# Performance work log

Measured on AMD Instinct MI355X. Metric: run time of the kernel, lower is better.

## Reference

```python
import jax, jax.numpy as jnp
import numpy as np

N_C, N_E, IN_FEAT, OUT_FEAT = 8192, 8192, 256, 128


def setup_inputs() -> dict:
    key = jax.random.key(0)
    ks = jax.random.split(key, 9)
    s = 1.0 / np.sqrt(IN_FEAT)
    return {
        "emb_cause": jax.random.normal(ks[0], (N_C, IN_FEAT), jnp.float32),
        "emb_effect": jax.random.normal(ks[1], (N_E, IN_FEAT), jnp.float32),
        "causal_mask": jax.random.randint(ks[2], (N_C, N_E), 0, 2, jnp.int32),
        "Wq": jax.random.uniform(ks[3], (IN_FEAT, OUT_FEAT), jnp.float32, -s, s),
        "bq": jax.random.uniform(ks[4], (OUT_FEAT,), jnp.float32, -s, s),
        "Wk": jax.random.uniform(ks[5], (IN_FEAT, OUT_FEAT), jnp.float32, -s, s),
        "bk": jax.random.uniform(ks[6], (OUT_FEAT,), jnp.float32, -s, s),
        "Wv": jax.random.uniform(ks[7], (IN_FEAT, OUT_FEAT), jnp.float32, -s, s),
        "bv": jax.random.uniform(ks[8], (OUT_FEAT,), jnp.float32, -s, s),
    }


def reference(emb_cause, emb_effect, causal_mask, Wq, bq, Wk, bk, Wv, bv):
    Q = emb_cause @ Wq + bq          # [N_c, D]
    K = emb_effect @ Wk + bk         # [N_e, D]
    V = emb_effect @ Wv + bv         # [N_e, D]
    scale = 1.0 / jnp.sqrt(jnp.asarray(Q.shape[-1], Q.dtype))
    scores = (Q @ K.T) * scale       # [N_c, N_e]
    scores = jnp.where(causal_mask == 0, -jnp.inf, scores)
    attn_weights = jax.nn.softmax(scores, axis=-1)
    causal_output = attn_weights @ V  # [N_c, D]
    return causal_output, attn_weights
```

## Files before the change

kernel.cpp:

```cpp
#include <hip/hip_runtime.h>

#define NC   8192
#define NEFF 8192
#define DIN  256
#define DOUT 128
#define SCALE 0.08838834764831843f

typedef float  f32x4  __attribute__((ext_vector_type(4)));
typedef short  s16x8  __attribute__((ext_vector_type(8)));
typedef unsigned long long u64;

__device__ __forceinline__ short f2bf(float f) {
    unsigned int u = __builtin_bit_cast(unsigned int, f);
    u += 0x7FFFu + ((u >> 16) & 1u);
    return (short)(u >> 16);
}

__device__ __forceinline__ s16x8 ld8(const short* p) {
    return *(const s16x8*)__builtin_assume_aligned(p, 16);
}

__device__ __forceinline__ unsigned getdw(int4 v, int i) {
    switch (i & 3) {
        case 0: return (unsigned)v.x;
        case 1: return (unsigned)v.y;
        case 2: return (unsigned)v.z;
        default: return (unsigned)v.w;
    }
}


__global__ __launch_bounds__(256, 2) void qkv_kernel(
    const float* __restrict__ embc, const float* __restrict__ embe,
    const float* __restrict__ Wq, const float* __restrict__ bq,
    const float* __restrict__ Wk, const float* __restrict__ bk,
    const float* __restrict__ Wv, const float* __restrict__ bv,
    short* __restrict__ Qf, short* __restrict__ Kf, short* __restrict__ Vf)
{
    const int mat = blockIdx.y;
    const float* src  = (mat == 0) ? embc : embe;
    const float* W    = (mat == 0) ? Wq : (mat == 1 ? Wk : Wv);
    const float* bias = (mat == 0) ? bq : (mat == 1 ? bk : bv);

    __shared__ short wt[DOUT][136];
    __shared__ short tbuf[4][16][132];
    __shared__ short tbufV[128][68];

    const int tid  = threadIdx.x;
    const int wave = tid >> 6, lane = tid & 63;
    const int quad = lane >> 4, ln16 = lane & 15;
    const int rowbase = blockIdx.x * 64;
    const int arow = rowbase + wave * 16 + ln16;

    f32x4 acc[8];
#pragma unroll
    for (int i = 0; i < 8; i++) acc[i] = (f32x4){0.f, 0.f, 0.f, 0.f};

    for (int h = 0; h < 2; h++) {
        __syncthreads();
        {
            const int n0 = (tid & 31) * 4;
            const int kb = tid >> 5;
#pragma unroll
            for (int i = 0; i < 16; i++) {
                const int k = kb + i * 8;
                const float4 w4 = *(const float4*)(W + (size_t)(h * 128 + k) * DOUT + n0);
                wt[n0 + 0][k] = f2bf(w4.x);
                wt[n0 + 1][k] = f2bf(w4.y);
                wt[n0 + 2][k] = f2bf(w4.z);
                wt[n0 + 3][k] = f2bf(w4.w);
            }
        }
        __syncthreads();

        s16x8 afr[4];
#pragma unroll
        for (int kc = 0; kc < 4; kc++) {
            const float* ap = src + (size_t)arow * DIN + h * 128 + kc * 32 + quad * 8;
            const float4 a0 = *(const float4*)ap;
            const float4 a1 = *(const float4*)(ap + 4);
            s16x8 a;
            a[0] = f2bf(a0.x); a[1] = f2bf(a0.y); a[2] = f2bf(a0.z); a[3] = f2bf(a0.w);
            a[4] = f2bf(a1.x); a[5] = f2bf(a1.y); a[6] = f2bf(a1.z); a[7] = f2bf(a1.w);
            afr[kc] = a;
        }
#pragma unroll
        for (int nt = 0; nt < 8; nt++) {
#pragma unroll
            for (int kc = 0; kc < 4; kc++) {
                const s16x8 b = ld8(&wt[nt * 16 + ln16][kc * 32 + quad * 8]);
                acc[nt] = __builtin_amdgcn_mfma_f32_16x16x32_bf16(afr[kc], b, acc[nt], 0, 0, 0);
            }
        }
    }

    if (mat < 2) {
        short* dst = (mat == 0) ? Qf : Kf;
        const float sc = (mat == 0) ? SCALE : 1.0f;
#pragma unroll
        for (int nt = 0; nt < 8; nt++) {
            const float bb = bias[nt * 16 + ln16];
#pragma unroll
            for (int r = 0; r < 4; r++)
                tbuf[wave][quad * 4 + r][nt * 16 + ln16] = f2bf((acc[nt][r] + bb) * sc);
        }
        const int tile = blockIdx.x * 4 + wave;
#pragma unroll
        for (int kc = 0; kc < 4; kc++) {
            const s16x8 fr = ld8(&tbuf[wave][ln16][kc * 32 + quad * 8]);
            *(s16x8*)(dst + ((size_t)(tile * 4 + kc) * 64 + lane) * 8) = fr;
        }
    } else {
#pragma unroll
        for (int nt = 0; nt < 8; nt++) {
            const float bb = bias[nt * 16 + ln16];
#pragma unroll
            for (int r = 0; r < 4; r++)
                tbufV[nt * 16 + ln16][wave * 16 + quad * 4 + r] = f2bf(acc[nt][r] + bb);
        }
        __syncthreads();
        const int ct = blockIdx.x >> 1;
        const int ksub0 = (blockIdx.x & 1) * 2;
        const int ks = wave & 1;
#pragma unroll
        for (int t = 0; t < 4; t++) {
            const int nt2 = (wave >> 1) * 4 + t;
            const s16x8 fr = ld8(&tbufV[nt2 * 16 + ln16][ks * 32 + quad * 8]);
            *(s16x8*)(Vf + ((size_t)((ct * 8 + nt2) * 4 + ksub0 + ks) * 64 + lane) * 8) = fr;
        }
    }
}

__global__ __launch_bounds__(256, 2) void stats_kernel(
    const int* __restrict__ mask, const short* __restrict__ Qf,
    const short* __restrict__ Kf, float* __restrict__ lsum,
    unsigned int* __restrict__ bm)
{
    __shared__ int4 bmbuf[4][32];

    const int bx = blockIdx.x, strip = blockIdx.y;
    const int tid  = threadIdx.x;
    const int wave = tid >> 6, lane = tid & 63;
    const int quad = lane >> 4, ln16 = lane & 15;
    const int rowbase = bx * 128 + wave * 32;
    const int t0 = rowbase >> 4;

    s16x8 aq[2][4];
#pragma unroll
    for (int rs = 0; rs < 2; rs++)
#pragma unroll
        for (int kc = 0; kc < 4; kc++)
            aq[rs][kc] = ld8(Qf + ((size_t)((t0 + rs) * 4 + kc) * 64 + lane) * 8);

    float lp[8] = {0.f, 0.f, 0.f, 0.f, 0.f, 0.f, 0.f, 0.f};

    for (int it = 0; it < 8; it++) {
        const int cb = strip * 1024 + it * 128;

        int4 mybm = {0, 0, 0, 0};
#pragma unroll 4
        for (int rr = 0; rr < 32; rr++) {
            const int* mrow = mask + (size_t)(rowbase + rr) * NEFF + cb;
            const int p0 = mrow[lane];
            const int p1 = mrow[64 + lane];
            const u64 b0 = __ballot(p0 != 0);
            const u64 b1 = __ballot(p1 != 0);
            int4 v;
            v.x = (int)(unsigned)(b0 & 0xffffffffull);
            v.y = (int)(unsigned)(b0 >> 32);
            v.z = (int)(unsigned)(b1 & 0xffffffffull);
            v.w = (int)(unsigned)(b1 >> 32);
            if (rr == lane) mybm = v;
        }
        if (lane < 32) {
            *(int4*)(bm + (size_t)(rowbase + lane) * 256 + (cb >> 5)) = mybm;
            bmbuf[wave][lane] = mybm;
        }
        int4 bmv[2][4];
#pragma unroll
        for (int rs = 0; rs < 2; rs++)
#pragma unroll
            for (int r = 0; r < 4; r++)
                bmv[rs][r] = bmbuf[wave][rs * 16 + quad * 4 + r];

#pragma unroll
        for (int nt = 0; nt < 8; nt++) {
            s16x8 bq[4];
#pragma unroll
            for (int kc = 0; kc < 4; kc++)
                bq[kc] = ld8(Kf + ((size_t)(((cb >> 4) + nt) * 4 + kc) * 64 + lane) * 8);
            f32x4 c0 = (f32x4){0.f, 0.f, 0.f, 0.f};
            f32x4 c1 = (f32x4){0.f, 0.f, 0.f, 0.f};
#pragma unroll
            for (int kc = 0; kc < 4; kc++) {
                c0 = __builtin_amdgcn_mfma_f32_16x16x32_bf16(aq[0][kc], bq[kc], c0, 0, 0, 0);
                c1 = __builtin_amdgcn_mfma_f32_16x16x32_bf16(aq[1][kc], bq[kc], c1, 0, 0, 0);
            }
#pragma unroll
            for (int rs = 0; rs < 2; rs++)
#pragma unroll
                for (int r = 0; r < 4; r++) {
                    const unsigned d = getdw(bmv[rs][r], nt >> 1);
                    const float cv = rs ? c1[r] : c0[r];
                    if ((d >> ((nt & 1) * 16 + ln16)) & 1u)
                        lp[rs * 4 + r] += __expf(cv);
                }
        }
    }

#pragma unroll
    for (int i = 0; i < 8; i++) {
        float v = lp[i];
        v += __shfl_xor(v, 1); v += __shfl_xor(v, 2);
        v += __shfl_xor(v, 4); v += __shfl_xor(v, 8);
        if (ln16 == 0)
            atomicAdd(&lsum[rowbase + (i >> 2) * 16 + quad * 4 + (i & 3)], v);
    }
}

__global__ __launch_bounds__(256, 2) void attn_kernel(
    const short* __restrict__ Qf, const short* __restrict__ Kf,
    const short* __restrict__ Vf, const float* __restrict__ lsum,
    const unsigned int* __restrict__ bm,
    float* __restrict__ outO, float* __restrict__ outW)
{
    __shared__ short wlds[4][32][132];

    const int bx = blockIdx.x, strip = blockIdx.y;
    const int tid  = threadIdx.x;
    const int wave = tid >> 6, lane = tid & 63;
    const int quad = lane >> 4, ln16 = lane & 15;
    const int rowbase = bx * 128 + wave * 32;
    const int t0 = rowbase >> 4;

    s16x8 aq[2][4];
#pragma unroll
    for (int rs = 0; rs < 2; rs++)
#pragma unroll
        for (int kc = 0; kc < 4; kc++)
            aq[rs][kc] = ld8(Qf + ((size_t)((t0 + rs) * 4 + kc) * 64 + lane) * 8);

    float rl[2][4];
#pragma unroll
    for (int rs = 0; rs < 2; rs++)
#pragma unroll
        for (int r = 0; r < 4; r++)
            rl[rs][r] = 1.0f / lsum[rowbase + rs * 16 + quad * 4 + r];

    f32x4 o[2][8];
#pragma unroll
    for (int rs = 0; rs < 2; rs++)
#pragma unroll
        for (int i = 0; i < 8; i++) o[rs][i] = (f32x4){0.f, 0.f, 0.f, 0.f};

    for (int it = 0; it < 8; it++) {
        const int cb = strip * 1024 + it * 128;

        int4 bmv[2][4];
#pragma unroll
        for (int rs = 0; rs < 2; rs++)
#pragma unroll
            for (int r = 0; r < 4; r++)
                bmv[rs][r] = *(const int4*)(bm + (size_t)(rowbase + rs * 16 + quad * 4 + r) * 256 + (cb >> 5));

#pragma unroll
        for (int nt = 0; nt < 8; nt++) {
            s16x8 bq[4];
#pragma unroll
            for (int kc = 0; kc < 4; kc++)
                bq[kc] = ld8(Kf + ((size_t)(((cb >> 4) + nt) * 4 + kc) * 64 + lane) * 8);
            f32x4 c0 = (f32x4){0.f, 0.f, 0.f, 0.f};
            f32x4 c1 = (f32x4){0.f, 0.f, 0.f, 0.f};
#pragma unroll
            for (int kc = 0; kc < 4; kc++) {
                c0 = __builtin_amdgcn_mfma_f32_16x16x32_bf16(aq[0][kc], bq[kc], c0, 0, 0, 0);
                c1 = __builtin_amdgcn_mfma_f32_16x16x32_bf16(aq[1][kc], bq[kc], c1, 0, 0, 0);
            }
#pragma unroll
            for (int rs = 0; rs < 2; rs++)
#pragma unroll
                for (int r = 0; r < 4; r++) {
                    const int row = rowbase + rs * 16 + quad * 4 + r;
                    const unsigned d = getdw(bmv[rs][r], nt >> 1);
                    const float cv = rs ? c1[r] : c0[r];
                    const float wv = ((d >> ((nt & 1) * 16 + ln16)) & 1u)
                                         ? __expf(cv) * rl[rs][r] : 0.0f;
                    outW[(size_t)row * NEFF + cb + nt * 16 + ln16] = wv;
                    wlds[wave][rs * 16 + quad * 4 + r][nt * 16 + ln16] = f2bf(wv);
                }
        }

#pragma unroll
        for (int ks = 0; ks < 4; ks++) {
            const s16x8 aw0 = ld8(&wlds[wave][ln16][ks * 32 + quad * 8]);
            const s16x8 aw1 = ld8(&wlds[wave][16 + ln16][ks * 32 + quad * 8]);
#pragma unroll
            for (int nt2 = 0; nt2 < 8; nt2++) {
                const s16x8 bv = ld8(Vf + ((size_t)(((cb >> 7) * 8 + nt2) * 4 + ks) * 64 + lane) * 8);
                o[0][nt2] = __builtin_amdgcn_mfma_f32_16x16x32_bf16(aw0, bv, o[0][nt2], 0, 0, 0);
                o[1][nt2] = __builtin_amdgcn_mfma_f32_16x16x32_bf16(aw1, bv, o[1][nt2], 0, 0, 0);
            }
        }
    }

#pragma unroll
    for (int rs = 0; rs < 2; rs++)
#pragma unroll
        for (int nt2 = 0; nt2 < 8; nt2++)
#pragma unroll
            for (int r = 0; r < 4; r++) {
                const int row = rowbase + rs * 16 + quad * 4 + r;
                atomicAdd(&outO[(size_t)row * DOUT + nt2 * 16 + ln16], o[rs][nt2][r]);
            }
}

extern "C" void kernel_launch(void* const* d_in, const int* in_sizes, int n_in,
                              void* d_out, int out_size, void* d_ws, size_t ws_size,
                              hipStream_t stream) {
    (void)in_sizes; (void)n_in; (void)out_size; (void)ws_size;

    const float* embc = (const float*)d_in[0];
    const float* embe = (const float*)d_in[1];
    const int*   mask = (const int*)d_in[2];
    const float* Wq = (const float*)d_in[3];
    const float* bq = (const float*)d_in[4];
    const float* Wk = (const float*)d_in[5];
    const float* bk = (const float*)d_in[6];
    const float* Wv = (const float*)d_in[7];
    const float* bv = (const float*)d_in[8];

    char* ws = (char*)d_ws;
    short* Qf = (short*)(ws);
    short* Kf = (short*)(ws + (2u << 20));
    short* Vf = (short*)(ws + (4u << 20));
    float* lsum = (float*)(ws + (6u << 20));
    unsigned int* bm = (unsigned int*)(ws + (8u << 20));

    float* outO = (float*)d_out;
    float* outW = outO + (size_t)NC * DOUT;

    hipMemsetAsync(lsum, 0, NC * sizeof(float), stream);
    hipMemsetAsync(outO, 0, (size_t)NC * DOUT * sizeof(float), stream);

    qkv_kernel<<<dim3(128, 3), 256, 0, stream>>>(embc, embe, Wq, bq, Wk, bk, Wv, bv,
                                                 Qf, Kf, Vf);
    stats_kernel<<<dim3(64, 8), 256, 0, stream>>>(mask, Qf, Kf, lsum, bm);
    attn_kernel<<<dim3(64, 8), 256, 0, stream>>>(Qf, Kf, Vf, lsum, bm, outO, outW);
}
```

Before: 728.1 us.

## Split mask bit-packing into a streaming kernel and raise grid parallelism

Mask bit-packing moves out of the stats kernel into a dedicated grid-stride pack kernel that reads the int mask coalesced and writes 64-bit ballot words. The stats kernel then reads packed bits and runs twice as many strips. The attention kernel halves rows per wave so the grid doubles and occupancy rises (launch bounds 4). This is meant to fix the strided row-wise mask reads and the low block count. The cost is an extra launch and per-block recomputation of K tiles across more blocks.

Result: faster. 652.2 us (-10.4%).

```diff
diff --git a/kernel.cpp b/kernel.cpp
--- a/kernel.cpp
+++ b/kernel.cpp
@@ -29,6 +29,26 @@
     }
 }
 
+
+__global__ __launch_bounds__(256) void pack_kernel(
+    const int* __restrict__ mask, u64* __restrict__ bm)
+{
+    const size_t stride = (size_t)gridDim.x * 256;
+    const size_t i0 = (size_t)blockIdx.x * 256 + threadIdx.x;
+    const bool lead = (threadIdx.x & 63) == 0;
+    for (size_t i = i0; i < (size_t)NC * NEFF; i += 8 * stride) {
+        int m[8];
+#pragma unroll
+        for (int j = 0; j < 8; j++) m[j] = mask[i + j * stride];
+        u64 b[8];
+#pragma unroll
+        for (int j = 0; j < 8; j++) b[j] = __ballot(m[j] != 0);
+        if (lead) {
+#pragma unroll
+            for (int j = 0; j < 8; j++) bm[(i + j * stride) >> 6] = b[j];
+        }
+    }
+}
 
 __global__ __launch_bounds__(256, 2) void qkv_kernel(
     const float* __restrict__ embc, const float* __restrict__ embe,
@@ -131,13 +151,10 @@
     }
 }
 
-__global__ __launch_bounds__(256, 2) void stats_kernel(
-    const int* __restrict__ mask, const short* __restrict__ Qf,
-    const short* __restrict__ Kf, float* __restrict__ lsum,
-    unsigned int* __restrict__ bm)
+__global__ __launch_bounds__(256, 4) void stats_kernel(
+    const unsigned int* __restrict__ bm, const short* __restrict__ Qf,
+    const short* __restrict__ Kf, float* __restrict__ lsum)
 {
-    __shared__ int4 bmbuf[4][32];
-
     const int bx = blockIdx.x, strip = blockIdx.y;
     const int tid  = threadIdx.x;
     const int wave = tid >> 6, lane = tid & 63;
@@ -154,34 +171,15 @@
 
     float lp[8] = {0.f, 0.f, 0.f, 0.f, 0.f, 0.f, 0.f, 0.f};
 
-    for (int it = 0; it < 8; it++) {
-        const int cb = strip * 1024 + it * 128;
-
-        int4 mybm = {0, 0, 0, 0};
-#pragma unroll 4
-        for (int rr = 0; rr < 32; rr++) {
-            const int* mrow = mask + (size_t)(rowbase + rr) * NEFF + cb;
-            const int p0 = mrow[lane];
-            const int p1 = mrow[64 + lane];
-            const u64 b0 = __ballot(p0 != 0);
-            const u64 b1 = __ballot(p1 != 0);
-            int4 v;
-            v.x = (int)(unsigned)(b0 & 0xffffffffull);
-            v.y = (int)(unsigned)(b0 >> 32);
-            v.z = (int)(unsigned)(b1 & 0xffffffffull);
-            v.w = (int)(unsigned)(b1 >> 32);
-            if (rr == lane) mybm = v;
-        }
-        if (lane < 32) {
-            *(int4*)(bm + (size_t)(rowbase + lane) * 256 + (cb >> 5)) = mybm;
-            bmbuf[wave][lane] = mybm;
-        }
+    for (int it = 0; it < 4; it++) {
+        const int cb = strip * 512 + it * 128;
+
         int4 bmv[2][4];
 #pragma unroll
         for (int rs = 0; rs < 2; rs++)
 #pragma unroll
             for (int r = 0; r < 4; r++)
-                bmv[rs][r] = bmbuf[wave][rs * 16 + quad * 4 + r];
+                bmv[rs][r] = *(const int4*)(bm + (size_t)(rowbase + rs * 16 + quad * 4 + r) * 256 + (cb >> 5));
 
 #pragma unroll
         for (int nt = 0; nt < 8; nt++) {
@@ -218,50 +216,42 @@
     }
 }
 
-__global__ __launch_bounds__(256, 2) void attn_kernel(
+__global__ __launch_bounds__(256, 4) void attn_kernel(
     const short* __restrict__ Qf, const short* __restrict__ Kf,
     const short* __restrict__ Vf, const float* __restrict__ lsum,
     const unsigned int* __restrict__ bm,
     float* __restrict__ outO, float* __restrict__ outW)
 {
-    __shared__ short wlds[4][32][132];
+    __shared__ short wlds[4][16][132];
 
     const int bx = blockIdx.x, strip = blockIdx.y;
     const int tid  = threadIdx.x;
     const int wave = tid >> 6, lane = tid & 63;
     const int quad = lane >> 4, ln16 = lane & 15;
-    const int rowbase = bx * 128 + wave * 32;
+    const int rowbase = bx * 64 + wave * 16;
     const int t0 = rowbase >> 4;
 
-    s16x8 aq[2][4];
-#pragma unroll
-    for (int rs = 0; rs < 2; rs++)
-#pragma unroll
-        for (int kc = 0; kc < 4; kc++)
-            aq[rs][kc] = ld8(Qf + ((size_t)((t0 + rs) * 4 + kc) * 64 + lane) * 8);
-
-    float rl[2][4];
-#pragma unroll
-    for (int rs = 0; rs < 2; rs++)
-#pragma unroll
-        for (int r = 0; r < 4; r++)
-            rl[rs][r] = 1.0f / lsum[rowbase + rs * 16 + quad * 4 + r];
-
-    f32x4 o[2][8];
-#pragma unroll
-    for (int rs = 0; rs < 2; rs++)
-#pragma unroll
-        for (int i = 0; i < 8; i++) o[rs][i] = (f32x4){0.f, 0.f, 0.f, 0.f};
+    s16x8 aq[4];
+#pragma unroll
+    for (int kc = 0; kc < 4; kc++)
+        aq[kc] = ld8(Qf + ((size_t)(t0 * 4 + kc) * 64 + lane) * 8);
+
+    float rl[4];
+#pragma unroll
+    for (int r = 0; r < 4; r++)
+        rl[r] = 1.0f / lsum[rowbase + quad * 4 + r];
+
+    f32x4 o[8];
+#pragma unroll
+    for (int i = 0; i < 8; i++) o[i] = (f32x4){0.f, 0.f, 0.f, 0.f};
 
     for (int it = 0; it < 8; it++) {
         const int cb = strip * 1024 + it * 128;
 
-        int4 bmv[2][4];
-#pragma unroll
-        for (int rs = 0; rs < 2; rs++)
-#pragma unroll
-            for (int r = 0; r < 4; r++)
-                bmv[rs][r] = *(const int4*)(bm + (size_t)(rowbase + rs * 16 + quad * 4 + r) * 256 + (cb >> 5));
+        int4 bmv[4];
+#pragma unroll
+        for (int r = 0; r < 4; r++)
+            bmv[r] = *(const int4*)(bm + (size_t)(rowbase + quad * 4 + r) * 256 + (cb >> 5));
 
 #pragma unroll
         for (int nt = 0; nt < 8; nt++) {
@@ -269,49 +259,39 @@
 #pragma unroll
             for (int kc = 0; kc < 4; kc++)
                 bq[kc] = ld8(Kf + ((size_t)(((cb >> 4) + nt) * 4 + kc) * 64 + lane) * 8);
-            f32x4 c0 = (f32x4){0.f, 0.f, 0.f, 0.f};
-            f32x4 c1 = (f32x4){0.f, 0.f, 0.f, 0.f};
-#pragma unroll
-            for (int kc = 0; kc < 4; kc++) {
-                c0 = __builtin_amdgcn_mfma_f32_16x16x32_bf16(aq[0][kc], bq[kc], c0, 0, 0, 0);
-                c1 = __builtin_amdgcn_mfma_f32_16x16x32_bf16(aq[1][kc], bq[kc], c1, 0, 0, 0);
-            }
-#pragma unroll
-            for (int rs = 0; rs < 2; rs++)
-#pragma unroll
-                for (int r = 0; r < 4; r++) {
-                    const int row = rowbase + rs * 16 + quad * 4 + r;
-                    const unsigned d = getdw(bmv[rs][r], nt >> 1);
-                    const float cv = rs ? c1[r] : c0[r];
-                    const float wv = ((d >> ((nt & 1) * 16 + ln16)) & 1u)
-                                         ? __expf(cv) * rl[rs][r] : 0.0f;
-                    outW[(size_t)row * NEFF + cb + nt * 16 + ln16] = wv;
-                    wlds[wave][rs * 16 + quad * 4 + r][nt * 16 + ln16] = f2bf(wv);
-                }
+            f32x4 c = (f32x4){0.f, 0.f, 0.f, 0.f};
+#pragma unroll
+            for (int kc = 0; kc < 4; kc++)
+                c = __builtin_amdgcn_mfma_f32_16x16x32_bf16(aq[kc], bq[kc], c, 0, 0, 0);
+#pragma unroll
+            for (int r = 0; r < 4; r++) {
+                const int row = rowbase + quad * 4 + r;
+                const unsigned d = getdw(bmv[r], nt >> 1);
+                const float wv = ((d >> ((nt & 1) * 16 + ln16)) & 1u)
+                                     ? __expf(c[r]) * rl[r] : 0.0f;
+                outW[(size_t)row * NEFF + cb + nt * 16 + ln16] = wv;
+                wlds[wave][quad * 4 + r][nt * 16 + ln16] = f2bf(wv);
+            }
         }
 
 #pragma unroll
         for (int ks = 0; ks < 4; ks++) {
-            const s16x8 aw0 = ld8(&wlds[wave][ln16][ks * 32 + quad * 8]);
-            const s16x8 aw1 = ld8(&wlds[wave][16 + ln16][ks * 32 + quad * 8]);
+            const s16x8 aw = ld8(&wlds[wave][ln16][ks * 32 + quad * 8]);
 #pragma unroll
             for (int nt2 = 0; nt2 < 8; nt2++) {
                 const s16x8 bv = ld8(Vf + ((size_t)(((cb >> 7) * 8 + nt2) * 4 + ks) * 64 + lane) * 8);
-                o[0][nt2] = __builtin_amdgcn_mfma_f32_16x16x32_bf16(aw0, bv, o[0][nt2], 0, 0, 0);
-                o[1][nt2] = __builtin_amdgcn_mfma_f32_16x16x32_bf16(aw1, bv, o[1][nt2], 0, 0, 0);
-            }
-        }
-    }
-
-#pragma unroll
-    for (int rs = 0; rs < 2; rs++)
-#pragma unroll
-        for (int nt2 = 0; nt2 < 8; nt2++)
-#pragma unroll
-            for (int r = 0; r < 4; r++) {
-                const int row = rowbase + rs * 16 + quad * 4 + r;
-                atomicAdd(&outO[(size_t)row * DOUT + nt2 * 16 + ln16], o[rs][nt2][r]);
-            }
+                o[nt2] = __builtin_amdgcn_mfma_f32_16x16x32_bf16(aw, bv, o[nt2], 0, 0, 0);
+            }
+        }
+    }
+
+#pragma unroll
+    for (int nt2 = 0; nt2 < 8; nt2++)
+#pragma unroll
+        for (int r = 0; r < 4; r++) {
+            const int row = rowbase + quad * 4 + r;
+            atomicAdd(&outO[(size_t)row * DOUT + nt2 * 16 + ln16], o[nt2][r]);
+        }
 }
 
 extern "C" void kernel_launch(void* const* d_in, const int* in_sizes, int n_in,
@@ -342,8 +322,9 @@
     hipMemsetAsync(lsum, 0, NC * sizeof(float), stream);
     hipMemsetAsync(outO, 0, (size_t)NC * DOUT * sizeof(float), stream);
 
+    pack_kernel<<<8192, 256, 0, stream>>>(mask, (u64*)bm);
     qkv_kernel<<<dim3(128, 3), 256, 0, stream>>>(embc, embe, Wq, bq, Wk, bk, Wv, bv,
                                                  Qf, Kf, Vf);
-    stats_kernel<<<dim3(64, 8), 256, 0, stream>>>(mask, Qf, Kf, lsum, bm);
-    attn_kernel<<<dim3(64, 8), 256, 0, stream>>>(Qf, Kf, Vf, lsum, bm, outO, outW);
-}
+    stats_kernel<<<dim3(64, 16), 256, 0, stream>>>(bm, Qf, Kf, lsum);
+    attn_kernel<<<dim3(128, 8), 256, 0, stream>>>(Qf, Kf, Vf, lsum, bm, outO, outW);
+}
```
